# Optimization experiments

Hardware: AMD Instinct MI355X
Metric: run time of the kernel (lower is better)

The kernel has to match this reference:

```python
import jax, jax.numpy as jnp
import numpy as np
from jax import lax

V_PATCH_NUMS = (1, 2, 3, 4, 5, 6, 8, 10, 13, 16)
SHARE_K = 4
RESI = 0.5  # abs(quant_resi)


def _area_matrix(pn, H):
    # F.interpolate(mode='area') == adaptive_avg_pool2d: uniform mean over [floor, ceil) window
    W = np.zeros((pn, H), np.float32)
    for i in range(pn):
        s = int(np.floor(i * H / pn)); e = int(np.ceil((i + 1) * H / pn))
        W[i, s:e] = 1.0 / (e - s)
    return W


def _cubic(x, a=-0.75):
    x = abs(x)
    if x <= 1.0:
        return (a + 2) * x**3 - (a + 3) * x**2 + 1
    if x < 2.0:
        return a * x**3 - 5 * a * x**2 + 8 * a * x - 4 * a
    return 0.0


def _bicubic_matrix(out, inp):
    # torch bicubic, align_corners=False, a=-0.75, border-clamped (separable 1D matrix)
    W = np.zeros((out, inp), np.float32)
    for i in range(out):
        src = (i + 0.5) * inp / out - 0.5
        i0 = int(np.floor(src)); t = src - i0
        for k in range(-1, 3):
            j = min(max(i0 + k, 0), inp - 1)
            W[i, j] += _cubic(k - t)
    return W


def _phi_select(si, SN, K=SHARE_K):
    ticks = np.linspace(1 / 3 / K, 1 - 1 / 3 / K, K) if K == 4 else np.linspace(1 / 2 / K, 1 - 1 / 2 / K, K)
    return int(np.argmin(np.abs(ticks - si / (SN - 1))))


def _phi(h, w, b):
    # Phi: h*(1-r) + conv3x3(h)*r
    y = lax.conv_general_dilated(h, w, (1, 1), 'SAME',
                                 dimension_numbers=('NCHW', 'OIHW', 'NCHW'))
    y = y + b[None, :, None, None]
    return h * (1.0 - RESI) + y * RESI


def reference(f, embedding, phi_w, phi_b):
    # Multi-scale residual vector quantization (VectorQuantizer2 hot path).
    # f: [B, C, 16, 16] latent; embedding: [V, C]; phi_w: [K, C, C, 3, 3]; phi_b: [K, C]
    B, C, H, Wd = f.shape
    SN = len(V_PATCH_NUMS)
    e2 = jnp.sum(embedding**2, axis=1)  # [V]
    f_hat = jnp.zeros_like(f)
    f_rest = f
    for si, pn in enumerate(V_PATCH_NUMS):
        if si != SN - 1:
            A = jnp.asarray(_area_matrix(pn, H))
            z = jnp.einsum('ph,bchw,qw->bcpq', A, f_rest, A)  # area downsample to pn x pn
        else:
            z = f_rest
        zf = z.transpose(0, 2, 3, 1).reshape(-1, C)  # [B*pn*pn, C]
        # squared-distance cdist + argmin codebook lookup
        d = jnp.sum(zf**2, axis=1, keepdims=True) - 2.0 * (zf @ embedding.T) + e2[None, :]
        idx = jnp.argmin(d, axis=1)  # [B*pn*pn]
        h = embedding[idx].reshape(B, pn, pn, C).transpose(0, 3, 1, 2)  # gather -> [B,C,pn,pn]
        if si != SN - 1:
            U = jnp.asarray(_bicubic_matrix(H, pn))
            h = jnp.einsum('hp,bcpq,wq->bchw', U, h, U)  # bicubic upsample to H x W
        k = _phi_select(si, SN)
        h = _phi(h, phi_w[k], phi_b[k])  # partially-shared Phi residual refinement
        f_hat = f_hat + h
        f_rest = f_rest - h
    return f_hat


def setup_inputs() -> dict:
    key = jax.random.key(0)
    k1, k2, k3 = jax.random.split(key, 3)
    f = jax.random.normal(k1, (64, 32, 16, 16), dtype=jnp.float32)
    embedding = jax.random.normal(k2, (4096, 32), dtype=jnp.float32)
    phi_w = jax.random.normal(k3, (4, 32, 32, 3, 3), dtype=jnp.float32) * 0.05
    phi_b = jnp.zeros((4, 32), dtype=jnp.float32)
    return {"f": f, "embedding": embedding, "phi_w": phi_w, "phi_b": phi_b}
```

## Files before the change

### kernel.cpp

```cpp
#include <hip/hip_runtime.h>
#include <cmath>


#define BB 64
#define CC 32
#define HH 16
#define VV 4096
#define NTOT (BB*CC*HH*HH)

typedef __attribute__((ext_vector_type(8))) short bf16x8;
typedef __attribute__((ext_vector_type(4))) float f32x4;

__device__ __forceinline__ double cubicw(double x) {
    x = fabs(x);
    const double a = -0.75;
    if (x <= 1.0) return ((a + 2.0) * x - (a + 3.0)) * x * x + 1.0;
    if (x < 2.0)  return (((a * x - 5.0 * a) * x + 8.0 * a) * x - 4.0 * a);
    return 0.0;
}

__device__ __forceinline__ unsigned int ordf(float d) {
    unsigned int b = __float_as_uint(d);
    return (b & 0x80000000u) ? ~b : (b | 0x80000000u);
}

__device__ __forceinline__ short f2bf(float x) {
    unsigned u = __float_as_uint(x);
    unsigned r = (u + 0x7fffu + ((u >> 16) & 1u)) >> 16;
    return (short)r;
}
__device__ __forceinline__ float bf2f(short h) {
    return __uint_as_float(((unsigned)(unsigned short)h) << 16);
}

__global__ void init_k(const float* __restrict__ f, const float* __restrict__ E,
                       float* __restrict__ f_rest, float* __restrict__ f_hat,
                       float* __restrict__ e2, float* __restrict__ z,
                       float* __restrict__ es) {
    int i = blockIdx.x * 256 + threadIdx.x;
    if (i < NTOT) { f_rest[i] = f[i]; f_hat[i] = 0.f; }
    if (i < VV) {
        float s = 0.f;
        unsigned short* ew = es ? (unsigned short*)(es + (size_t)i * 48) : (unsigned short*)0;
        #pragma unroll
        for (int c = 0; c < CC; ++c) {
            float x = E[i * CC + c];
            s += x * x;
            if (ew) {
                short h = f2bf(x); float rm = x - bf2f(h);
                short m = f2bf(rm); float rl = rm - bf2f(m);
                short l = f2bf(rl);
                ew[c] = (unsigned short)h;
                ew[32 + c] = (unsigned short)m;
                ew[64 + c] = (unsigned short)l;
            }
        }
        e2[i] = s;
    }
    if (i < BB * CC) {
        const float* src = f + (size_t)i * (HH * HH);
        float s = 0.f;
        for (int j = 0; j < HH * HH; ++j) s += src[j];
        z[i] = s * (1.0f / 256.0f);
    }
}

__global__ __launch_bounds__(256, 4) void argsmall_k(const float* __restrict__ z,
        const float* __restrict__ E, const float* __restrict__ e2,
        unsigned long long* __restrict__ bestk, int M, int G, int gsz) {
    const int t = threadIdx.x;
    int m = blockIdx.x * 64 + (t & 63);
    int w = __builtin_amdgcn_readfirstlane(t >> 6);
    int wg = blockIdx.y * 4 + w;
    int v0 = wg * gsz;
    float zr[CC]; float z2 = 0.f;
    const float4* zp = (const float4*)(z + (size_t)m * CC);
    #pragma unroll
    for (int c4 = 0; c4 < 8; ++c4) {
        float4 v = zp[c4];
        zr[c4*4+0] = v.x; zr[c4*4+1] = v.y; zr[c4*4+2] = v.z; zr[c4*4+3] = v.w;
        z2 += v.x*v.x + v.y*v.y + v.z*v.z + v.w*v.w;
    }
    const float* e = E + (size_t)v0 * CC;
    float best = 3.4e38f; int bv = v0;
    for (int v = v0; v < v0 + gsz; v += 2, e += 2 * CC) {
        float a0 = 0.f, a1 = 0.f, b0 = 0.f, b1 = 0.f;
        #pragma unroll
        for (int c = 0; c < CC; c += 2) {
            a0 = fmaf(zr[c],   e[c],      a0);
            a1 = fmaf(zr[c+1], e[c+1],    a1);
            b0 = fmaf(zr[c],   e[CC+c],   b0);
            b1 = fmaf(zr[c+1], e[CC+c+1], b1);
        }
        float dA = fmaf(-2.f, a0 + a1, z2 + e2[v]);
        float dB = fmaf(-2.f, b0 + b1, z2 + e2[v+1]);
        if (dA < best) { best = dA; bv = v; }
        if (dB < best) { best = dB; bv = v + 1; }
    }
    bestk[(size_t)m * G + wg] = ((unsigned long long)ordf(best) << 32) |
                                (unsigned long long)(unsigned int)bv;
}

__global__ __launch_bounds__(256, 4) void argmf_k(const unsigned short* __restrict__ zs,
        const float* __restrict__ es, const float* __restrict__ e2,
        unsigned long long* __restrict__ bestk, int M, int G, int gsz) {
    __shared__ float s_es[128 * 52];
    __shared__ float s_e2[128];
    const int t = threadIdx.x;
    const int g = blockIdx.y;
    const int v0 = g * gsz;
    for (int i = t; i < gsz * 12; i += 256) {
        int row = i / 12, part = i - row * 12;
        *(float4*)&s_es[row * 52 + part * 4] =
            *(const float4*)&es[(size_t)(v0 + row) * 48 + part * 4];
    }
    for (int i = t; i < gsz; i += 256) s_e2[i] = e2[v0 + i];

    const int lane = t & 63;
    const int w = t >> 6;
    const int n = lane & 15, kq = lane >> 4;

    int tb[2]; bf16x8 ah[2], am[2], al[2];
    #pragma unroll
    for (int pt = 0; pt < 2; ++pt) {
        int tb0 = blockIdx.x * 128 + w * 32 + pt * 16;
        if (tb0 > M - 16) tb0 = M - 16;
        tb[pt] = tb0;
        const unsigned short* zp = zs + (size_t)(tb0 + n) * 96 + kq * 8;
        ah[pt] = *(const bf16x8*)(zp);
        am[pt] = *(const bf16x8*)(zp + 32);
        al[pt] = *(const bf16x8*)(zp + 64);
    }
    __syncthreads();

    float bd[2][4]; int bc[2][4];
    #pragma unroll
    for (int pt = 0; pt < 2; ++pt)
        #pragma unroll
        for (int r = 0; r < 4; ++r) { bd[pt][r] = 3.4e38f; bc[pt][r] = 0; }

    const int nct = gsz >> 4;
    for (int ct = 0; ct < nct; ++ct) {
        int base = (ct * 16 + n) * 52 + kq * 4;
        bf16x8 eh = *(const bf16x8*)&s_es[base];
        bf16x8 em = *(const bf16x8*)&s_es[base + 16];
        bf16x8 el = *(const bf16x8*)&s_es[base + 32];
        float e2c = s_e2[ct * 16 + n];
        #pragma unroll
        for (int pt = 0; pt < 2; ++pt) {
            f32x4 Ca = {0.f, 0.f, 0.f, 0.f};
            f32x4 Cb = {e2c, e2c, e2c, e2c};
            Ca = __builtin_amdgcn_mfma_f32_16x16x32_bf16(ah[pt], eh, Ca, 0, 0, 0);
            Cb = __builtin_amdgcn_mfma_f32_16x16x32_bf16(am[pt], eh, Cb, 0, 0, 0);
            Ca = __builtin_amdgcn_mfma_f32_16x16x32_bf16(ah[pt], em, Ca, 0, 0, 0);
            Cb = __builtin_amdgcn_mfma_f32_16x16x32_bf16(al[pt], eh, Cb, 0, 0, 0);
            Ca = __builtin_amdgcn_mfma_f32_16x16x32_bf16(ah[pt], el, Ca, 0, 0, 0);
            Cb = __builtin_amdgcn_mfma_f32_16x16x32_bf16(am[pt], em, Cb, 0, 0, 0);
            #pragma unroll
            for (int r = 0; r < 4; ++r) {
                float d = Ca[r] + Cb[r];
                if (d < bd[pt][r]) { bd[pt][r] = d; bc[pt][r] = ct; }
            }
        }
    }
    #pragma unroll
    for (int pt = 0; pt < 2; ++pt) {
        #pragma unroll
        for (int r = 0; r < 4; ++r) {
            int v = v0 + bc[pt][r] * 16 + n;
            unsigned long long k = ((unsigned long long)ordf(bd[pt][r]) << 32) |
                                   (unsigned long long)(unsigned int)v;
            #pragma unroll
            for (int msk = 1; msk < 16; msk <<= 1) {
                unsigned long long o = __shfl_xor(k, msk);
                if (o < k) k = o;
            }
            if (n == 0)
                bestk[(size_t)(tb[pt] + kq * 4 + r) * G + g] = k;
        }
    }
}

__global__ __launch_bounds__(256, 4) void argbig_k(const float* __restrict__ z,
        const float* __restrict__ E, const float* __restrict__ e2,
        unsigned long long* __restrict__ bestk, int M, int G, int gsz) {
    __shared__ float s_e[128 * CC];
    __shared__ float s_e2[128];
    const int T = gridDim.x * 256;
    const int g = blockIdx.y;
    const int v0 = g * gsz;
    {
        const float4* src = (const float4*)(E + (size_t)v0 * CC);
        float4* dst = (float4*)s_e;
        for (int i = threadIdx.x; i < gsz * 8; i += 256) dst[i] = src[i];
        if (threadIdx.x < gsz) s_e2[threadIdx.x] = e2[v0 + threadIdx.x];
    }
    int   mm[2];
    bool  act[2];
    float zr[2][CC];
    float z2[2];
    #pragma unroll
    for (int pt = 0; pt < 2; ++pt) {
        int m0 = blockIdx.x * 256 + threadIdx.x + pt * T;
        act[pt] = (m0 < M);
        int m = act[pt] ? m0 : M - 1;
        mm[pt] = m;
        const float4* zp = (const float4*)(z + (size_t)m * CC);
        float zz = 0.f;
        #pragma unroll
        for (int c4 = 0; c4 < 8; ++c4) {
            float4 v = zp[c4];
            zr[pt][c4*4+0] = v.x; zr[pt][c4*4+1] = v.y;
            zr[pt][c4*4+2] = v.z; zr[pt][c4*4+3] = v.w;
            zz += v.x*v.x + v.y*v.y + v.z*v.z + v.w*v.w;
        }
        z2[pt] = zz;
    }
    __syncthreads();
    float best[2]; int bv[2];
    #pragma unroll
    for (int pt = 0; pt < 2; ++pt) { best[pt] = 3.4e38f; bv[pt] = v0; }
    const float4* ev = (const float4*)s_e;
    for (int vi = 0; vi < gsz; ++vi, ev += 8) {
        float4 e0 = ev[0], e1 = ev[1], e2v = ev[2], e3 = ev[3];
        float4 e4 = ev[4], e5 = ev[5], e6v = ev[6], e7 = ev[7];
        float ef[CC] = {e0.x,e0.y,e0.z,e0.w, e1.x,e1.y,e1.z,e1.w,
                        e2v.x,e2v.y,e2v.z,e2v.w, e3.x,e3.y,e3.z,e3.w,
                        e4.x,e4.y,e4.z,e4.w, e5.x,e5.y,e5.z,e5.w,
                        e6v.x,e6v.y,e6v.z,e6v.w, e7.x,e7.y,e7.z,e7.w};
        float a0 = 0.f, a1 = 0.f, b0 = 0.f, b1 = 0.f;
        #pragma unroll
        for (int c = 0; c < CC; c += 2) {
            a0 = fmaf(zr[0][c],   ef[c],   a0);
            a1 = fmaf(zr[0][c+1], ef[c+1], a1);
            b0 = fmaf(zr[1][c],   ef[c],   b0);
            b1 = fmaf(zr[1][c+1], ef[c+1], b1);
        }
        float e2c = s_e2[vi];
        float dA = fmaf(-2.f, a0 + a1, z2[0] + e2c);
        float dB = fmaf(-2.f, b0 + b1, z2[1] + e2c);
        int v = v0 + vi;
        if (dA < best[0]) { best[0] = dA; bv[0] = v; }
        if (dB < best[1]) { best[1] = dB; bv[1] = v; }
    }
    #pragma unroll
    for (int pt = 0; pt < 2; ++pt)
        if (act[pt])
            bestk[(size_t)mm[pt] * G + g] =
                ((unsigned long long)ordf(best[pt]) << 32) |
                (unsigned long long)(unsigned int)bv[pt];
}

__global__ __launch_bounds__(512) void fuse_k(const unsigned long long* __restrict__ bestk,
                      const float* __restrict__ E,
                      const float* __restrict__ pw, const float* __restrict__ pb,
                      float* __restrict__ f_hat, float* __restrict__ f_rest,
                      float* __restrict__ z_next, unsigned short* __restrict__ zsn,
                      int pn, int G, int TPP, int kphi, int pnn) {
    __shared__ float s_buf[CC * 18 * 20];
    __shared__ float s_pw[CC * 3 * 4 * 8];
    __shared__ float s_part[3 * 128 * 20];
    __shared__ int   s_idx[256];
    __shared__ float s_w[HH][4];
    __shared__ int   s_j[HH][4];
    __shared__ unsigned long long s_red[512];
    const int t   = threadIdx.x;
    const int cog = blockIdx.x;
    const int b   = blockIdx.y;
    const int P   = pn * pn;
    const int half = t >> 8;
    const int tl   = t & 255;

    {
        int p = t / TPP, sub = t - p * TPP;
        unsigned long long bk = ~0ull;
        if (p < P) {
            const unsigned long long* kp = bestk + (size_t)(b * P + p) * G;
            for (int gg = sub; gg < G; gg += TPP) {
                unsigned long long o = kp[gg];
                if (o < bk) bk = o;
            }
        }
        s_red[t] = bk;
        __syncthreads();
        for (int s = TPP >> 1; s > 0; s >>= 1) {
            if ((sub < s) && p < P) {
                unsigned long long o = s_red[t + s];
                if (o < s_red[t]) s_red[t] = o;
            }
            __syncthreads();
        }
        if (t < P) s_idx[t] = (int)(unsigned int)(s_red[t * TPP] & 0xffffffffull);
    }
    if (t < HH) {
        double src = (t + 0.5) * (double)pn / 16.0 - 0.5;
        double fi = floor(src); int i0 = (int)fi; double tt = src - fi;
        #pragma unroll
        for (int k = 0; k < 4; ++k) {
            int j = i0 - 1 + k; j = j < 0 ? 0 : (j > pn - 1 ? pn - 1 : j);
            s_j[t][k] = j;
            s_w[t][k] = (float)cubicw((double)(k - 1) - tt);
        }
    }
    {
        const float* src = pw + ((size_t)(kphi * CC + cog * 8)) * CC * 9;
        for (int i = t; i < 8 * CC * 9; i += 512) {
            int l  = i / (CC * 9);
            int r  = i - l * (CC * 9);
            int ci = r / 9; int kk = r - ci * 9;
            int kh = kk / 3; int kw = kk - kh * 3;
            int cp = l >> 1, ce = l & 1;
            s_pw[ci * 96 + kh * 32 + cp * 8 + ce * 4 + kw] = src[i];
        }
    }
    __syncthreads();

    if (tl < HH * pn) {
        int h = tl / pn, q = tl % pn;
        int cbase = half * 16;
        float acc[16];
        #pragma unroll
        for (int c = 0; c < 16; ++c) acc[c] = 0.f;
        #pragma unroll
        for (int k = 0; k < 4; ++k) {
            float wv = s_w[h][k];
            if (wv == 0.0f) continue;
            int row = s_idx[s_j[h][k] * pn + q];
            const float4* er = (const float4*)(E + (size_t)row * CC + cbase);
            #pragma unroll
            for (int c4 = 0; c4 < 4; ++c4) {
                float4 e4 = er[c4];
                acc[c4*4+0] = fmaf(wv, e4.x, acc[c4*4+0]);
                acc[c4*4+1] = fmaf(wv, e4.y, acc[c4*4+1]);
                acc[c4*4+2] = fmaf(wv, e4.z, acc[c4*4+2]);
                acc[c4*4+3] = fmaf(wv, e4.w, acc[c4*4+3]);
            }
        }
        #pragma unroll
        for (int c = 0; c < 16; ++c)
            s_buf[((cbase + c) * HH + h) * pn + q] = acc[c];
    }
    __syncthreads();

    {
        int h = tl >> 4, w = tl & 15;
        int cbase = half * 16;
        float acc[16];
        #pragma unroll
        for (int c = 0; c < 16; ++c) acc[c] = 0.f;
        #pragma unroll
        for (int k = 0; k < 4; ++k) {
            float wh = s_w[w][k];
            int j = s_j[w][k];
            #pragma unroll
            for (int c = 0; c < 16; ++c)
                acc[c] = fmaf(wh, s_buf[((cbase + c) * HH + h) * pn + j], acc[c]);
        }
        __syncthreads();
        #pragma unroll
        for (int c = 0; c < 16; ++c)
            s_buf[((cbase + c) * 18 + h + 1) * 20 + w + 1] = acc[c];
        if (w == 0) {
            #pragma unroll
            for (int c = 0; c < 16; ++c) s_buf[((cbase + c) * 18 + h + 1) * 20] = 0.f;
        }
        if (w >= 13) {
            #pragma unroll
            for (int c = 0; c < 16; ++c) s_buf[((cbase + c) * 18 + h + 1) * 20 + w + 4] = 0.f;
        }
        if (h == 0) {
            #pragma unroll
            for (int c = 0; c < 16; ++c) {
                s_buf[((cbase + c) * 18) * 20 + w] = 0.f;
                if (w < 4) s_buf[((cbase + c) * 18) * 20 + 16 + w] = 0.f;
            }
        }
        if (h == 15) {
            #pragma unroll
            for (int c = 0; c < 16; ++c) {
                s_buf[((cbase + c) * 18 + 17) * 20 + w] = 0.f;
                if (w < 4) s_buf[((cbase + c) * 18 + 17) * 20 + 16 + w] = 0.f;
            }
        }
    }
    __syncthreads();

    const int cp  = tl >> 6;
    const int q   = (tl >> 5) & 1;
    const int s   = tl & 31;
    const int h   = s >> 1;
    const int w0  = (s & 1) * 8;
    const int wid = half * 2 + q;
    const int pos = cp * 32 + s;
    float accE[8], accO[8];
    #pragma unroll
    for (int o = 0; o < 8; ++o) { accE[o] = 0.f; accO[o] = 0.f; }
    const int ci0 = wid * 8;
    for (int ci = ci0; ci < ci0 + 8; ++ci) {
        const float* wrow = &s_pw[ci * 96 + cp * 8];
        #pragma unroll
        for (int kk = 0; kk < 3; ++kk) {
            int kh = kk + q; kh = (kh >= 3) ? kh - 3 : kh;
            const float4* xr = (const float4*)&s_buf[(ci * 18 + h + kh) * 20 + w0];
            float4 a0 = xr[0], a1 = xr[1], a2 = xr[2];
            float xf[12] = {a0.x, a0.y, a0.z, a0.w, a1.x, a1.y, a1.z, a1.w,
                            a2.x, a2.y, a2.z, a2.w};
            const float4* wp = (const float4*)(wrow + kh * 32);
            float4 wA = wp[0];
            float4 wB = wp[1];
            #pragma unroll
            for (int o = 0; o < 8; ++o) {
                accE[o] += xf[o] * wA.x + xf[o+1] * wA.y + xf[o+2] * wA.z;
                accO[o] += xf[o] * wB.x + xf[o+1] * wB.y + xf[o+2] * wB.z;
            }
        }
    }
    if (wid != 0) {
        float* dst = &s_part[((wid - 1) * 128 + pos) * 20];
        *(float4*)(dst +  0) = make_float4(accE[0], accE[1], accE[2], accE[3]);
        *(float4*)(dst +  4) = make_float4(accE[4], accE[5], accE[6], accE[7]);
        *(float4*)(dst +  8) = make_float4(accO[0], accO[1], accO[2], accO[3]);
        *(float4*)(dst + 12) = make_float4(accO[4], accO[5], accO[6], accO[7]);
    }
    __syncthreads();

    float4 rE0, rE1, rO0, rO1;
    if (wid == 0) {
        #pragma unroll
        for (int g2 = 0; g2 < 3; ++g2) {
            const float* sp = &s_part[(g2 * 128 + pos) * 20];
            float4 p0 = *(const float4*)(sp + 0), p1 = *(const float4*)(sp + 4);
            float4 p2 = *(const float4*)(sp + 8), p3 = *(const float4*)(sp + 12);
            accE[0] += p0.x; accE[1] += p0.y; accE[2] += p0.z; accE[3] += p0.w;
            accE[4] += p1.x; accE[5] += p1.y; accE[6] += p1.z; accE[7] += p1.w;
            accO[0] += p2.x; accO[1] += p2.y; accO[2] += p2.z; accO[3] += p2.w;
            accO[4] += p3.x; accO[5] += p3.y; accO[6] += p3.z; accO[7] += p3.w;
        }
        float biasE = pb[kphi * CC + cog * 8 + cp * 2];
        float biasO = pb[kphi * CC + cog * 8 + cp * 2 + 1];
        #pragma unroll
        for (int o = 0; o < 8; ++o) { accE[o] += biasE; accO[o] += biasO; }
        #pragma unroll
        for (int c = 0; c < 2; ++c) {
            const float* acc = c ? accO : accE;
            int co = cog * 8 + cp * 2 + c;
            float hf[8];
            #pragma unroll
            for (int o = 0; o < 8; ++o) {
                float hv = s_buf[(co * 18 + h + 1) * 20 + w0 + o + 1];
                hf[o] = 0.5f * hv + 0.5f * acc[o];
            }
            size_t base = ((size_t)(b * CC + co) * HH + h) * HH + w0;
            float4* fh = (float4*)(f_hat + base);
            float4* fr = (float4*)(f_rest + base);
            float4 v0 = fh[0], v1 = fh[1];
            v0.x += hf[0]; v0.y += hf[1]; v0.z += hf[2]; v0.w += hf[3];
            v1.x += hf[4]; v1.y += hf[5]; v1.z += hf[6]; v1.w += hf[7];
            fh[0] = v0; fh[1] = v1;
            float4 r0 = fr[0], r1 = fr[1];
            r0.x -= hf[0]; r0.y -= hf[1]; r0.z -= hf[2]; r0.w -= hf[3];
            r1.x -= hf[4]; r1.y -= hf[5]; r1.z -= hf[6]; r1.w -= hf[7];
            fr[0] = r0; fr[1] = r1;
            if (c) { rO0 = r0; rO1 = r1; } else { rE0 = r0; rE1 = r1; }
        }
    }

    if (pnn > 0) {
        __syncthreads();
        float* fn = s_buf;
        if (wid == 0) {
            #pragma unroll
            for (int c = 0; c < 2; ++c) {
                int cl = cp * 2 + c;
                float* d = &fn[(cl * HH + h) * HH + w0];
                float4 r0 = c ? rO0 : rE0, r1 = c ? rO1 : rE1;
                d[0] = r0.x; d[1] = r0.y; d[2] = r0.z; d[3] = r0.w;
                d[4] = r1.x; d[5] = r1.y; d[6] = r1.z; d[7] = r1.w;
            }
        }
        __syncthreads();
        int P2 = pnn * pnn;
        for (int i = t; i < P2 * 8; i += 512) {
            int cl = i & 7, pq = i >> 3;
            int q2 = pq % pnn, p2 = pq / pnn;
            int sp = (p2 * HH) / pnn, ep = ((p2 + 1) * HH + pnn - 1) / pnn;
            int sq = (q2 * HH) / pnn, eq = ((q2 + 1) * HH + pnn - 1) / pnn;
            float wgt = 1.0f / ((float)(ep - sp) * (float)(eq - sq));
            float sum = 0.f;
            for (int h2 = sp; h2 < ep; ++h2)
                for (int w2 = sq; w2 < eq; ++w2)
                    sum += fn[(cl * HH + h2) * HH + w2];
            float v = sum * wgt;
            int c = cog * 8 + cl;
            if (zsn) {
                float tv = -2.0f * v;
                size_t baz = (size_t)(b * P2 + pq) * 96 + c;
                unsigned short hh = (unsigned short)f2bf(tv);
                float rm = tv - bf2f((short)hh);
                unsigned short mm2 = (unsigned short)f2bf(rm);
                float rl = rm - bf2f((short)mm2);
                unsigned short ll = (unsigned short)f2bf(rl);
                zsn[baz] = hh; zsn[baz + 32] = mm2; zsn[baz + 64] = ll;
            } else {
                z_next[((size_t)(b * P2 + pq)) * CC + c] = v;
            }
        }
    }
}

extern "C" void kernel_launch(void* const* d_in, const int* in_sizes, int n_in,
                              void* d_out, int out_size, void* d_ws, size_t ws_size,
                              hipStream_t stream) {
    const float* f  = (const float*)d_in[0];
    const float* E  = (const float*)d_in[1];
    const float* pw = (const float*)d_in[2];
    const float* pb = (const float*)d_in[3];
    float* out = (float*)d_out;

    const size_t need_base = (size_t)(NTOT + VV) * 4 + (size_t)524288 * 8 +
                             (size_t)524288 * 4;
    const size_t need_mf = need_base + (size_t)VV * 48 * 4 +
                           (size_t)16384 * 96 * 2;
    const bool use_mf = (ws_size >= need_mf);

    float* wsf    = (float*)d_ws;
    float* f_rest = wsf;
    float* e2     = wsf + (size_t)NTOT;
    unsigned long long* bestk = (unsigned long long*)(e2 + VV);
    float* z      = (float*)(bestk + 524288);
    float* es     = use_mf ? (z + 524288) : (float*)0;
    unsigned short* zs = use_mf ? (unsigned short*)(es + (size_t)VV * 48) : (unsigned short*)0;

    int phik[10];
    {
        double start = 1.0 / 3.0 / 4.0;
        double stop  = 1.0 - 1.0 / 3.0 / 4.0;
        double step  = (stop - start) / 3.0;
        double ticks[4];
        for (int i = 0; i < 4; ++i) ticks[i] = (double)i * step + start;
        ticks[3] = stop;
        for (int si = 0; si < 10; ++si) {
            double s = (double)si / 9.0;
            int bk = 0; double bd = fabs(ticks[0] - s);
            for (int tq = 1; tq < 4; ++tq) {
                double d2 = fabs(ticks[tq] - s);
                if (d2 < bd) { bd = d2; bk = tq; }
            }
            phik[si] = bk;
        }
    }

    static const int pns[10]  = {1, 2, 3, 4, 5, 6, 8, 10, 13, 16};
    static const int grpS[10] = {256, 128, 64, 32, 32, 16, 0, 0, 0, 0};
    static const int grpF[10] = {0, 0, 0, 0, 0, 0, 128, 64, 32, 32};
    static const int grpM[10] = {0, 0, 0, 0, 0, 0, 32, 32, 32, 32};

    init_k<<<(NTOT + 255) / 256, 256, 0, stream>>>(f, E, f_rest, out, e2, z, es);

    for (int si = 0; si < 10; ++si) {
        int pn = pns[si];
        int P = pn * pn;
        int M = BB * P;
        int G, TPP;
        if (pn <= 6) {
            int grp = grpS[si];
            G = grp * 4;
            int gsz = VV / G;
            argsmall_k<<<dim3(P, grp), 256, 0, stream>>>(z, E, e2, bestk, M, G, gsz);
        } else if (use_mf) {
            G = grpM[si];
            int gsz = VV / G;
            int bx = (M + 127) / 128;
            argmf_k<<<dim3(bx, G), 256, 0, stream>>>(zs, es, e2, bestk, M, G, gsz);
        } else {
            G = grpF[si];
            int gsz = VV / G;
            int bx = (M + 511) / 512;
            argbig_k<<<dim3(bx, G), 256, 0, stream>>>(z, E, e2, bestk, M, G, gsz);
        }
        TPP = 1;
        while (TPP * 2 * P <= 512) TPP *= 2;
        int pnn = (si < 9) ? pns[si + 1] : 0;
        unsigned short* zsn = (pnn >= 8 && use_mf) ? zs : (unsigned short*)0;
        fuse_k<<<dim3(4, BB), 512, 0, stream>>>(bestk, E, pw, pb,
                                                out, f_rest, z, zsn,
                                                pn, G, TPP, phik[si], pnn);
    }
}
```

Measured before the change: 416.2 us.

## Pre-tile split-bf16 codebook for direct MFMA loads and extend MFMA path to small scales

The codebook's hi/mid/lo bf16 split is now stored in an MFMA-fragment-tiled layout, so argmf_k reads each fragment straight from global memory instead of staging it in shared memory and synchronising. The MFMA argmin path is also extended to scales with patch sizes 4-6, and the codebook group counts per scale are reduced so each block scans more codes. This removes the LDS staging and barrier and moves the mid-size scales onto matrix cores, at the cost of relying on cache hits for the repeated global codebook reads and using fewer blocks on the large scales.

```diff
diff --git a/kernel.cpp b/kernel.cpp
--- a/kernel.cpp
+++ b/kernel.cpp
@@ -36,23 +36,24 @@
 __global__ void init_k(const float* __restrict__ f, const float* __restrict__ E,
                        float* __restrict__ f_rest, float* __restrict__ f_hat,
                        float* __restrict__ e2, float* __restrict__ z,
-                       float* __restrict__ es) {
+                       unsigned short* __restrict__ est) {
     int i = blockIdx.x * 256 + threadIdx.x;
     if (i < NTOT) { f_rest[i] = f[i]; f_hat[i] = 0.f; }
     if (i < VV) {
         float s = 0.f;
-        unsigned short* ew = es ? (unsigned short*)(es + (size_t)i * 48) : (unsigned short*)0;
+        int tile = i >> 4, n = i & 15;
         #pragma unroll
         for (int c = 0; c < CC; ++c) {
             float x = E[i * CC + c];
             s += x * x;
-            if (ew) {
+            if (est) {
                 short h = f2bf(x); float rm = x - bf2f(h);
                 short m = f2bf(rm); float rl = rm - bf2f(m);
                 short l = f2bf(rl);
-                ew[c] = (unsigned short)h;
-                ew[32 + c] = (unsigned short)m;
-                ew[64 + c] = (unsigned short)l;
+                int idx = tile * 1536 + (n * 4 + (c >> 3)) * 8 + (c & 7);
+                est[idx]        = (unsigned short)h;
+                est[idx + 512]  = (unsigned short)m;
+                est[idx + 1024] = (unsigned short)l;
             }
         }
         e2[i] = s;
@@ -102,20 +103,11 @@
 }
 
 __global__ __launch_bounds__(256, 4) void argmf_k(const unsigned short* __restrict__ zs,
-        const float* __restrict__ es, const float* __restrict__ e2,
+        const unsigned short* __restrict__ est, const float* __restrict__ e2,
         unsigned long long* __restrict__ bestk, int M, int G, int gsz) {
-    __shared__ float s_es[128 * 52];
-    __shared__ float s_e2[128];
     const int t = threadIdx.x;
     const int g = blockIdx.y;
     const int v0 = g * gsz;
-    for (int i = t; i < gsz * 12; i += 256) {
-        int row = i / 12, part = i - row * 12;
-        *(float4*)&s_es[row * 52 + part * 4] =
-            *(const float4*)&es[(size_t)(v0 + row) * 48 + part * 4];
-    }
-    for (int i = t; i < gsz; i += 256) s_e2[i] = e2[v0 + i];
-
     const int lane = t & 63;
     const int w = t >> 6;
     const int n = lane & 15, kq = lane >> 4;
@@ -131,7 +123,6 @@
         am[pt] = *(const bf16x8*)(zp + 32);
         al[pt] = *(const bf16x8*)(zp + 64);
     }
-    __syncthreads();
 
     float bd[2][4]; int bc[2][4];
     #pragma unroll
@@ -140,12 +131,14 @@
         for (int r = 0; r < 4; ++r) { bd[pt][r] = 3.4e38f; bc[pt][r] = 0; }
 
     const int nct = gsz >> 4;
-    for (int ct = 0; ct < nct; ++ct) {
-        int base = (ct * 16 + n) * 52 + kq * 4;
-        bf16x8 eh = *(const bf16x8*)&s_es[base];
-        bf16x8 em = *(const bf16x8*)&s_es[base + 16];
-        bf16x8 el = *(const bf16x8*)&s_es[base + 32];
-        float e2c = s_e2[ct * 16 + n];
+    const unsigned short* ep = est + (size_t)(v0 >> 4) * 1536 +
+                               (size_t)(n * 4 + kq) * 8;
+    const float* e2p = e2 + v0 + n;
+    for (int ct = 0; ct < nct; ++ct, ep += 1536, e2p += 16) {
+        bf16x8 eh = *(const bf16x8*)(ep);
+        bf16x8 em = *(const bf16x8*)(ep + 512);
+        bf16x8 el = *(const bf16x8*)(ep + 1024);
+        float e2c = *e2p;
         #pragma unroll
         for (int pt = 0; pt < 2; ++pt) {
             f32x4 Ca = {0.f, 0.f, 0.f, 0.f};
@@ -519,7 +512,7 @@
 
     const size_t need_base = (size_t)(NTOT + VV) * 4 + (size_t)524288 * 8 +
                              (size_t)524288 * 4;
-    const size_t need_mf = need_base + (size_t)VV * 48 * 4 +
+    const size_t need_mf = need_base + (size_t)VV * 96 * 2 +
                            (size_t)16384 * 96 * 2;
     const bool use_mf = (ws_size >= need_mf);
 
@@ -528,8 +521,8 @@
     float* e2     = wsf + (size_t)NTOT;
     unsigned long long* bestk = (unsigned long long*)(e2 + VV);
     float* z      = (float*)(bestk + 524288);
-    float* es     = use_mf ? (z + 524288) : (float*)0;
-    unsigned short* zs = use_mf ? (unsigned short*)(es + (size_t)VV * 48) : (unsigned short*)0;
+    unsigned short* est = use_mf ? (unsigned short*)(z + 524288) : (unsigned short*)0;
+    unsigned short* zs  = use_mf ? (est + (size_t)VV * 96) : (unsigned short*)0;
 
     int phik[10];
     {
@@ -553,16 +546,17 @@
     static const int pns[10]  = {1, 2, 3, 4, 5, 6, 8, 10, 13, 16};
     static const int grpS[10] = {256, 128, 64, 32, 32, 16, 0, 0, 0, 0};
     static const int grpF[10] = {0, 0, 0, 0, 0, 0, 128, 64, 32, 32};
-    static const int grpM[10] = {0, 0, 0, 0, 0, 0, 32, 32, 32, 32};
-
-    init_k<<<(NTOT + 255) / 256, 256, 0, stream>>>(f, E, f_rest, out, e2, z, es);
+    static const int grpM[10] = {0, 0, 0, 32, 32, 32, 16, 16, 8, 8};
+
+    init_k<<<(NTOT + 255) / 256, 256, 0, stream>>>(f, E, f_rest, out, e2, z, est);
 
     for (int si = 0; si < 10; ++si) {
         int pn = pns[si];
         int P = pn * pn;
         int M = BB * P;
         int G, TPP;
-        if (pn <= 6) {
+        bool small_path = use_mf ? (pn <= 3) : (pn <= 6);
+        if (small_path) {
             int grp = grpS[si];
             G = grp * 4;
             int gsz = VV / G;
@@ -571,7 +565,7 @@
             G = grpM[si];
             int gsz = VV / G;
             int bx = (M + 127) / 128;
-            argmf_k<<<dim3(bx, G), 256, 0, stream>>>(zs, es, e2, bestk, M, G, gsz);
+            argmf_k<<<dim3(bx, G), 256, 0, stream>>>(zs, est, e2, bestk, M, G, gsz);
         } else {
             G = grpF[si];
             int gsz = VV / G;
@@ -581,7 +575,7 @@
         TPP = 1;
         while (TPP * 2 * P <= 512) TPP *= 2;
         int pnn = (si < 9) ? pns[si + 1] : 0;
-        unsigned short* zsn = (pnn >= 8 && use_mf) ? zs : (unsigned short*)0;
+        unsigned short* zsn = (pnn >= 4 && use_mf) ? zs : (unsigned short*)0;
         fuse_k<<<dim3(4, BB), 512, 0, stream>>>(bestk, E, pw, pb,
                                                 out, f_rest, z, zsn,
                                                 pn, G, TPP, phik[si], pnn);
```

After: 392.0 us. -5.8%, faster.
